# Kernel tuning notes

Hardware: AMD Instinct MI355X
Metric: run time of the kernel (lower is better)

Reference implementation:

```python
import jax, jax.numpy as jnp
import numpy as np

EMBED_DIM = 1024
PROJ_DIM = 128
B = 32
S = 1024


def setup_inputs() -> dict:
    key = jax.random.key(0)
    k1, k2, k3 = jax.random.split(key, 3)
    context = jax.random.normal(k1, (S, B, EMBED_DIM), jnp.float32)  # [seq, batch, embed]
    prior = jax.random.uniform(k2, (B, S), dtype=jnp.float32)
    padding_mask = jnp.zeros((B, S), jnp.int32)
    # xavier_uniform for proj_weight [2*proj_dim, embed_dim]
    bound = float(np.sqrt(6.0 / (2 * PROJ_DIM + EMBED_DIM)))
    proj_weight = jax.random.uniform(k3, (2 * PROJ_DIM, EMBED_DIM), jnp.float32, -bound, bound)
    proj_bias = jnp.zeros((2 * PROJ_DIM,), jnp.float32)
    return {"context": context, "prior": prior, "padding_mask": padding_mask,
            "proj_weight": proj_weight, "proj_bias": proj_bias}


def reference(context, prior, padding_mask, proj_weight, proj_bias):
    ctx = jnp.transpose(context, (1, 0, 2))  # [B, S, E]
    b, s, e = ctx.shape
    qk = ctx @ proj_weight.T + proj_bias  # [B, S, 2*proj_dim]
    query, key = jnp.split(qk, 2, axis=2)
    # neighbor scores (note: original divides by embed_dim, not proj_dim)
    fwd = jnp.sum(query[:, :-1] * key[:, 1:], axis=-1) / e    # [B, S-1]
    bwd = jnp.sum(query[:, 1:] * key[:, :-1], axis=-1) / e    # [B, S-1]
    ninf = jnp.full((b, 1), -jnp.inf, ctx.dtype)
    col0 = jnp.concatenate([fwd, ninf], axis=1)   # score[:, :, 0]
    col1 = jnp.concatenate([ninf, bwd], axis=1)   # score[:, :, 1]
    rolled_mask = jnp.roll(padding_mask, -1, axis=1)
    col0 = jnp.where(rolled_mask == 1, -jnp.inf, col0)
    prob = jax.nn.softmax(jnp.stack([col0, col1], axis=-1), axis=-1)  # [B, S, 2]
    # torch .roll with no dims flattens first -- replicate exactly
    shift_prob = jnp.roll(prob[:, :, 1].reshape(-1), -1).reshape(b, s)
    p = jnp.sqrt(prob[:, :, 0] * shift_prob + 1e-6)
    neighbor_attn = prior + (1 - prior) * p  # [B, S]
    log_prob = jnp.log(neighbor_attn)
    log_prob = jnp.where(rolled_mask == 1, 0.0, log_prob)
    # The two triangular bmms compute C[i,j] = sum_{k=i}^{j-1} log_prob[k] for j>i.
    # Equivalent O(S^2) form via exclusive prefix sum of log_prob[:, :-1].
    csp = jnp.concatenate([jnp.zeros((b, 1), ctx.dtype),
                           jnp.cumsum(log_prob[:, :-1], axis=1)], axis=1)  # [B, S]
    diff = csp[:, None, :] - csp[:, :, None]  # diff[b,i,j] = csp[j] - csp[i]
    upper = jnp.triu(diff, k=1)
    constituent_attn = jnp.exp(upper + jnp.swapaxes(upper, 1, 2))
    constituent_attn = jnp.where(jnp.eye(s, dtype=bool), 0.0, constituent_attn)
    return constituent_attn, neighbor_attn
```

## Files before the change

kernel.cpp:

```cpp
#include <hip/hip_runtime.h>
#include <hip/hip_bf16.h>
#include <math.h>

#define EMB 1024
#define BATCH 32
#define SEQ 1024
#define J2 256
#define BM 64
#define BN 256
#define BK 64
#define NIT (EMB / BK)
#define PSEL 0x07060302u

typedef __attribute__((ext_vector_type(8))) short short8;
typedef __attribute__((ext_vector_type(4))) float f32x4;
typedef const __attribute__((address_space(1))) void gvoid;
typedef __attribute__((address_space(3))) void lvoid;

__device__ __forceinline__ unsigned bcast(float f) {
    union { float f; unsigned u; } c; c.f = f; return c.u;
}
__device__ __forceinline__ unsigned pack_bf16(float f0, float f1) {
    return __builtin_amdgcn_perm(bcast(f1) + 0x8000u, bcast(f0) + 0x8000u, PSEL);
}

__global__ __launch_bounds__(256) void convw(const float* __restrict__ W,
                                             __hip_bfloat16* __restrict__ Wb) {
    int i = blockIdx.x * 256 + threadIdx.x;
    float4 v = ((const float4*)W)[i];
    __hip_bfloat16 h[4];
    h[0] = __float2bfloat16(v.x); h[1] = __float2bfloat16(v.y);
    h[2] = __float2bfloat16(v.z); h[3] = __float2bfloat16(v.w);
    *(short4*)&Wb[i * 4] = *(short4*)h;
}

__global__ __launch_bounds__(256) void gemm_mfma(const float* __restrict__ ctx,
                                                 const __hip_bfloat16* __restrict__ Wb,
                                                 const float* __restrict__ bias,
                                                 __hip_bfloat16* __restrict__ qkb) {
    __shared__ __align__(16) __hip_bfloat16 As[2 * BM * BK];
    __shared__ __align__(16) __hip_bfloat16 Bs[2 * BN * BK];
    const int t = threadIdx.x;
    const int lane = t & 63, w = t >> 6;
    const int m0 = blockIdx.x * BM;
    const int wn = w * 64;
    const int lm = lane & 15, lq = lane >> 4;

    f32x4 acc[4][4] = {};

    float bv[4];
    #pragma unroll
    for (int ni = 0; ni < 4; ni++) bv[ni] = bias[wn + ni * 16 + lm];

    const float4* ctx4 = (const float4*)ctx;
    const int ar0 = t >> 3, ak = t & 7;
    const int ar1 = 32 + ar0;
    const int as0 = (ak ^ (ar0 & 7)) * 8;
    const int as1 = (ak ^ (ar1 & 7)) * 8;
    const size_t abase0 = (size_t)(m0 + ar0) * 256 + ak * 2;
    const size_t abase1 = (size_t)(m0 + ar1) * 256 + ak * 2;

    #pragma unroll
    for (int c = 0; c < 8; c++) {
        int li = c * 256 + t, row = li >> 3;
        int k8 = (li & 7) ^ (row & 7);
        __builtin_amdgcn_global_load_lds(
            (gvoid*)(Wb + (size_t)row * EMB + k8 * 8),
            (lvoid*)&Bs[(c * 256 + w * 64) * 8], 16, 0, 0);
    }
    float4 v0a = ctx4[abase0], v0b = ctx4[abase0 + 1];
    float4 v1a = ctx4[abase1], v1b = ctx4[abase1 + 1];
    {
        uint4 p0, p1;
        p0.x = pack_bf16(v0a.x, v0a.y); p0.y = pack_bf16(v0a.z, v0a.w);
        p0.z = pack_bf16(v0b.x, v0b.y); p0.w = pack_bf16(v0b.z, v0b.w);
        p1.x = pack_bf16(v1a.x, v1a.y); p1.y = pack_bf16(v1a.z, v1a.w);
        p1.z = pack_bf16(v1b.x, v1b.y); p1.w = pack_bf16(v1b.z, v1b.w);
        *(uint4*)&As[ar0 * BK + as0] = p0;
        *(uint4*)&As[ar1 * BK + as1] = p1;
    }
    v0a = ctx4[abase0 + 16]; v0b = ctx4[abase0 + 17];
    v1a = ctx4[abase1 + 16]; v1b = ctx4[abase1 + 17];
    asm volatile("s_waitcnt vmcnt(0) lgkmcnt(0)" ::: "memory");
    __builtin_amdgcn_s_barrier();

    for (int it = 0; it < NIT; ++it) {
        const int cur = it & 1;
        const __hip_bfloat16* Ac = As + cur * (BM * BK);
        const __hip_bfloat16* Bc = Bs + cur * (BN * BK);
        __hip_bfloat16* An = As + (cur ^ 1) * (BM * BK);
        __hip_bfloat16* Bn = Bs + (cur ^ 1) * (BN * BK);
        const bool stage = (it + 1 < NIT);
        const bool pre   = (it + 2 < NIT);
        if (stage) {
            uint4 p0, p1;
            p0.x = pack_bf16(v0a.x, v0a.y); p0.y = pack_bf16(v0a.z, v0a.w);
            p0.z = pack_bf16(v0b.x, v0b.y); p0.w = pack_bf16(v0b.z, v0b.w);
            p1.x = pack_bf16(v1a.x, v1a.y); p1.y = pack_bf16(v1a.z, v1a.w);
            p1.z = pack_bf16(v1b.x, v1b.y); p1.w = pack_bf16(v1b.z, v1b.w);
            *(uint4*)&An[ar0 * BK + as0] = p0;
            *(uint4*)&An[ar1 * BK + as1] = p1;
            const int k0n = (it + 1) * BK;
            #pragma unroll
            for (int c = 0; c < 8; c++) {
                int li = c * 256 + t, row = li >> 3;
                int k8 = (li & 7) ^ (row & 7);
                __builtin_amdgcn_global_load_lds(
                    (gvoid*)(Wb + (size_t)row * EMB + k0n + k8 * 8),
                    (lvoid*)&Bn[(c * 256 + w * 64) * 8], 16, 0, 0);
            }
            if (pre) {
                const size_t ko = (size_t)(it + 2) * (BK / 4);
                v0a = ctx4[abase0 + ko]; v0b = ctx4[abase0 + ko + 1];
                v1a = ctx4[abase1 + ko]; v1b = ctx4[abase1 + ko + 1];
            }
        }
        #pragma unroll
        for (int kk = 0; kk < BK; kk += 32) {
            const int off = ((((kk >> 5) << 2) + lq) ^ (lm & 7)) * 8;
            short8 af[4], bfr[4];
            #pragma unroll
            for (int i = 0; i < 4; i++) {
                af[i]  = *(const short8*)&Ac[(i * 16 + lm) * BK + off];
                bfr[i] = *(const short8*)&Bc[(wn + i * 16 + lm) * BK + off];
            }
            #pragma unroll
            for (int mi = 0; mi < 4; mi++)
                #pragma unroll
                for (int ni = 0; ni < 4; ni++)
                    acc[mi][ni] = __builtin_amdgcn_mfma_f32_16x16x32_bf16(
                        af[mi], bfr[ni], acc[mi][ni], 0, 0, 0);
        }
        if (stage) {
            asm volatile("s_waitcnt vmcnt(0) lgkmcnt(0)" ::: "memory");
            __builtin_amdgcn_s_barrier();
        }
    }

    #pragma unroll
    for (int mi = 0; mi < 4; mi++) {
        #pragma unroll
        for (int r = 0; r < 4; r++) {
            int m = m0 + mi * 16 + lq * 4 + r;
            int s = m >> 5, b = m & 31;
            __hip_bfloat16* orow = qkb + (size_t)((b << 10) + s) * J2;
            #pragma unroll
            for (int ni = 0; ni < 4; ni++) {
                int n = wn + ni * 16 + lm;
                orow[n] = __float2bfloat16(acc[mi][ni][r] + bv[ni]);
            }
        }
    }
}

__global__ __launch_bounds__(256) void scores(const __hip_bfloat16* __restrict__ qkb,
                                              float* __restrict__ fwd,
                                              float* __restrict__ bwd) {
    int wave = threadIdx.x >> 6, lane = threadIdx.x & 63;
    int idx = blockIdx.x * 4 + wave;
    int s = idx & (SEQ - 1);
    if (s == SEQ - 1) return;
    const unsigned* r0 = (const unsigned*)(qkb + (size_t)idx * J2);
    const unsigned* r1 = r0 + 128;
    unsigned q0 = r0[lane], k0 = r0[64 + lane];
    unsigned q1 = r1[lane], k1 = r1[64 + lane];
    float2 q0f = __bfloat1622float2(*(const __hip_bfloat162*)&q0);
    float2 k0f = __bfloat1622float2(*(const __hip_bfloat162*)&k0);
    float2 q1f = __bfloat1622float2(*(const __hip_bfloat162*)&q1);
    float2 k1f = __bfloat1622float2(*(const __hip_bfloat162*)&k1);
    float f = q0f.x * k1f.x + q0f.y * k1f.y;
    float w = q1f.x * k0f.x + q1f.y * k0f.y;
    #pragma unroll
    for (int off = 32; off; off >>= 1) {
        f += __shfl_xor(f, off);
        w += __shfl_xor(w, off);
    }
    if (lane == 0) {
        fwd[idx] = f * (1.f / 1024.f);
        bwd[idx] = w * (1.f / 1024.f);
    }
}

__global__ __launch_bounds__(1024) void neighbor(const float* __restrict__ fwd,
                                                 const float* __restrict__ bwd,
                                                 const float* __restrict__ prior,
                                                 const int* __restrict__ mask,
                                                 float* __restrict__ out_n,
                                                 float* __restrict__ csp) {
    int b = blockIdx.x, s = threadIdx.x;
    int lane = s & 63, w = s >> 6;
    __shared__ float p1s[SEQ];
    __shared__ float incl[SEQ];
    __shared__ float wsum[16];
    int base = b << 10;
    int rolled = mask[base + ((s + 1) & (SEQ - 1))];
    float c0 = (s < SEQ - 1) ? fwd[base + s] : -INFINITY;
    if (rolled) c0 = -INFINITY;
    float c1 = (s > 0) ? bwd[base + s - 1] : -INFINITY;
    float m = fmaxf(c0, c1);
    float e0 = expf(c0 - m), e1 = expf(c1 - m);
    float inv = 1.f / (e0 + e1);
    float p0 = e0 * inv, p1 = e1 * inv;
    p1s[s] = p1;
    __syncthreads();
    float shift = (s < SEQ - 1) ? p1s[s + 1] : 0.f;
    float p = sqrtf(p0 * shift + 1e-6f);
    float pr = prior[base + s];
    float na = pr + (1.f - pr) * p;
    out_n[base + s] = na;
    float lp = logf(na);
    if (rolled) lp = 0.f;
    float x = lp;
    #pragma unroll
    for (int off = 1; off < 64; off <<= 1) {
        float v = __shfl_up(x, off);
        if (lane >= off) x += v;
    }
    if (lane == 63) wsum[w] = x;
    __syncthreads();
    if (w == 0) {
        float v = (lane < 16) ? wsum[lane] : 0.f;
        #pragma unroll
        for (int off = 1; off < 16; off <<= 1) {
            float t2 = __shfl_up(v, off);
            if (lane >= off) v += t2;
        }
        if (lane < 16) wsum[lane] = v;
    }
    __syncthreads();
    float woff = (w > 0) ? wsum[w - 1] : 0.f;
    incl[s] = x + woff;
    __syncthreads();
    csp[base + s] = (s == 0) ? 0.f : incl[s - 1];
}

__global__ __launch_bounds__(256) void outk(const float* __restrict__ csp,
                                            float* __restrict__ out) {
    int blk = blockIdx.x;
    int b = blk >> 7, i0 = (blk & 127) << 3;
    const float* crow = csp + (b << 10);
    int t = threadIdx.x;
    float4 cj = ((const float4*)crow)[t];
    int j0 = t << 2;
    float4* o4 = (float4*)(out + ((size_t)(b << 10) + i0) * SEQ) + t;
    #pragma unroll
    for (int r = 0; r < 8; r++) {
        int i = i0 + r;
        float ci = crow[i];
        float4 v; float d;
        d = (j0 + 0 > i) ? cj.x - ci : ci - cj.x;
        v.x = (j0 + 0 == i) ? 0.f : __expf(d);
        d = (j0 + 1 > i) ? cj.y - ci : ci - cj.y;
        v.y = (j0 + 1 == i) ? 0.f : __expf(d);
        d = (j0 + 2 > i) ? cj.z - ci : ci - cj.z;
        v.z = (j0 + 2 == i) ? 0.f : __expf(d);
        d = (j0 + 3 > i) ? cj.w - ci : ci - cj.w;
        v.w = (j0 + 3 == i) ? 0.f : __expf(d);
        o4[r * 256] = v;
    }
}

extern "C" void kernel_launch(void* const* d_in, const int* in_sizes, int n_in,
                              void* d_out, int out_size, void* d_ws, size_t ws_size,
                              hipStream_t stream) {
    (void)in_sizes; (void)n_in; (void)out_size; (void)ws_size;
    const float* ctx   = (const float*)d_in[0];
    const float* prior = (const float*)d_in[1];
    const int*   mask  = (const int*)d_in[2];
    const float* W     = (const float*)d_in[3];
    const float* bias  = (const float*)d_in[4];
    float* out = (float*)d_out;
    float* ws  = (float*)d_ws;

    __hip_bfloat16* qkb = (__hip_bfloat16*)ws;
    float* fwd = ws + 4194304;
    float* bwd = fwd + 32768;
    float* csp = bwd + 32768;
    __hip_bfloat16* Wb = (__hip_bfloat16*)(csp + 32768);
    float* out_n = out + (size_t)BATCH * SEQ * SEQ;

    convw    <<<256, 256, 0, stream>>>(W, Wb);
    gemm_mfma<<<(BATCH * SEQ) / BM, 256, 0, stream>>>(ctx, Wb, bias, qkb);
    scores   <<<(BATCH * SEQ) / 4, 256, 0, stream>>>(qkb, fwd, bwd);
    neighbor <<<BATCH, 1024, 0, stream>>>(fwd, bwd, prior, mask, out_n, csp);
    outk     <<<(BATCH * SEQ) / 8, 256, 0, stream>>>(csp, out);
}
```

Measured before the change: 269.3 us.

## Read weight fragments directly from global memory instead of staging in LDS

The B operand (bf16 weight) is no longer staged through shared memory with global_load_lds. Each wave now loads its MFMA B fragments straight from global memory, which is expected to hit in L2 since the weight is small and shared by all blocks. The A prefetch distance also drops from two stages to one, and the barrier now waits only on LDS traffic. This cuts LDS use from about 80KB to 16KB, allowing more blocks per CU, but it exposes global-load latency right before the MFMAs and removes the deeper prefetch.

```diff
diff --git a/kernel.cpp b/kernel.cpp
--- a/kernel.cpp
+++ b/kernel.cpp
@@ -14,8 +14,6 @@
 
 typedef __attribute__((ext_vector_type(8))) short short8;
 typedef __attribute__((ext_vector_type(4))) float f32x4;
-typedef const __attribute__((address_space(1))) void gvoid;
-typedef __attribute__((address_space(3))) void lvoid;
 
 __device__ __forceinline__ unsigned bcast(float f) {
     union { float f; unsigned u; } c; c.f = f; return c.u;
@@ -39,7 +37,6 @@
                                                  const float* __restrict__ bias,
                                                  __hip_bfloat16* __restrict__ qkb) {
     __shared__ __align__(16) __hip_bfloat16 As[2 * BM * BK];
-    __shared__ __align__(16) __hip_bfloat16 Bs[2 * BN * BK];
     const int t = threadIdx.x;
     const int lane = t & 63, w = t >> 6;
     const int m0 = blockIdx.x * BM;
@@ -51,6 +48,10 @@
     float bv[4];
     #pragma unroll
     for (int ni = 0; ni < 4; ni++) bv[ni] = bias[wn + ni * 16 + lm];
+
+    const __hip_bfloat16* bp[4];
+    #pragma unroll
+    for (int ni = 0; ni < 4; ni++) bp[ni] = Wb + (size_t)(wn + ni * 16 + lm) * EMB;
 
     const float4* ctx4 = (const float4*)ctx;
     const int ar0 = t >> 3, ak = t & 7;
@@ -60,17 +61,9 @@
     const size_t abase0 = (size_t)(m0 + ar0) * 256 + ak * 2;
     const size_t abase1 = (size_t)(m0 + ar1) * 256 + ak * 2;
 
-    #pragma unroll
-    for (int c = 0; c < 8; c++) {
-        int li = c * 256 + t, row = li >> 3;
-        int k8 = (li & 7) ^ (row & 7);
-        __builtin_amdgcn_global_load_lds(
-            (gvoid*)(Wb + (size_t)row * EMB + k8 * 8),
-            (lvoid*)&Bs[(c * 256 + w * 64) * 8], 16, 0, 0);
-    }
-    float4 v0a = ctx4[abase0], v0b = ctx4[abase0 + 1];
-    float4 v1a = ctx4[abase1], v1b = ctx4[abase1 + 1];
     {
+        float4 v0a = ctx4[abase0], v0b = ctx4[abase0 + 1];
+        float4 v1a = ctx4[abase1], v1b = ctx4[abase1 + 1];
         uint4 p0, p1;
         p0.x = pack_bf16(v0a.x, v0a.y); p0.y = pack_bf16(v0a.z, v0a.w);
         p0.z = pack_bf16(v0b.x, v0b.y); p0.w = pack_bf16(v0b.z, v0b.w);
@@ -79,19 +72,38 @@
         *(uint4*)&As[ar0 * BK + as0] = p0;
         *(uint4*)&As[ar1 * BK + as1] = p1;
     }
-    v0a = ctx4[abase0 + 16]; v0b = ctx4[abase0 + 17];
-    v1a = ctx4[abase1 + 16]; v1b = ctx4[abase1 + 17];
-    asm volatile("s_waitcnt vmcnt(0) lgkmcnt(0)" ::: "memory");
+    asm volatile("s_waitcnt lgkmcnt(0)" ::: "memory");
     __builtin_amdgcn_s_barrier();
 
     for (int it = 0; it < NIT; ++it) {
         const int cur = it & 1;
         const __hip_bfloat16* Ac = As + cur * (BM * BK);
-        const __hip_bfloat16* Bc = Bs + cur * (BN * BK);
         __hip_bfloat16* An = As + (cur ^ 1) * (BM * BK);
-        __hip_bfloat16* Bn = Bs + (cur ^ 1) * (BN * BK);
         const bool stage = (it + 1 < NIT);
-        const bool pre   = (it + 2 < NIT);
+        const int k0 = it * BK;
+        float4 v0a, v0b, v1a, v1b;
+        if (stage) {
+            const size_t ko = (size_t)(it + 1) * (BK / 4);
+            v0a = ctx4[abase0 + ko]; v0b = ctx4[abase0 + ko + 1];
+            v1a = ctx4[abase1 + ko]; v1b = ctx4[abase1 + ko + 1];
+        }
+        #pragma unroll
+        for (int kk = 0; kk < BK; kk += 32) {
+            const int off = ((((kk >> 5) << 2) + lq) ^ (lm & 7)) * 8;
+            const int bo = k0 + kk + lq * 8;
+            short8 af[4], bfr[4];
+            #pragma unroll
+            for (int i = 0; i < 4; i++) {
+                af[i]  = *(const short8*)&Ac[(i * 16 + lm) * BK + off];
+                bfr[i] = *(const short8*)(bp[i] + bo);
+            }
+            #pragma unroll
+            for (int mi = 0; mi < 4; mi++)
+                #pragma unroll
+                for (int ni = 0; ni < 4; ni++)
+                    acc[mi][ni] = __builtin_amdgcn_mfma_f32_16x16x32_bf16(
+                        af[mi], bfr[ni], acc[mi][ni], 0, 0, 0);
+        }
         if (stage) {
             uint4 p0, p1;
             p0.x = pack_bf16(v0a.x, v0a.y); p0.y = pack_bf16(v0a.z, v0a.w);
@@ -100,39 +112,7 @@
             p1.z = pack_bf16(v1b.x, v1b.y); p1.w = pack_bf16(v1b.z, v1b.w);
             *(uint4*)&An[ar0 * BK + as0] = p0;
             *(uint4*)&An[ar1 * BK + as1] = p1;
-            const int k0n = (it + 1) * BK;
-            #pragma unroll
-            for (int c = 0; c < 8; c++) {
-                int li = c * 256 + t, row = li >> 3;
-                int k8 = (li & 7) ^ (row & 7);
-                __builtin_amdgcn_global_load_lds(
-                    (gvoid*)(Wb + (size_t)row * EMB + k0n + k8 * 8),
-                    (lvoid*)&Bn[(c * 256 + w * 64) * 8], 16, 0, 0);
-            }
-            if (pre) {
-                const size_t ko = (size_t)(it + 2) * (BK / 4);
-                v0a = ctx4[abase0 + ko]; v0b = ctx4[abase0 + ko + 1];
-                v1a = ctx4[abase1 + ko]; v1b = ctx4[abase1 + ko + 1];
-            }
-        }
-        #pragma unroll
-        for (int kk = 0; kk < BK; kk += 32) {
-            const int off = ((((kk >> 5) << 2) + lq) ^ (lm & 7)) * 8;
-            short8 af[4], bfr[4];
-            #pragma unroll
-            for (int i = 0; i < 4; i++) {
-                af[i]  = *(const short8*)&Ac[(i * 16 + lm) * BK + off];
-                bfr[i] = *(const short8*)&Bc[(wn + i * 16 + lm) * BK + off];
-            }
-            #pragma unroll
-            for (int mi = 0; mi < 4; mi++)
-                #pragma unroll
-                for (int ni = 0; ni < 4; ni++)
-                    acc[mi][ni] = __builtin_amdgcn_mfma_f32_16x16x32_bf16(
-                        af[mi], bfr[ni], acc[mi][ni], 0, 0, 0);
-        }
-        if (stage) {
-            asm volatile("s_waitcnt vmcnt(0) lgkmcnt(0)" ::: "memory");
+            asm volatile("s_waitcnt lgkmcnt(0)" ::: "memory");
             __builtin_amdgcn_s_barrier();
         }
     }
```

Measured after the change: 275.7 us. 1.02x slower.

## Halve GEMM tile to BM=32, BK=32 with in-loop A prefetch

Applied to the files above, without the earlier changes.

Shrinks the projection GEMM tile from 64 to 32 rows and the K step from 64 to 32, with a new LDS swizzle for 4 chunks per row. This doubles the number of blocks to fill more CUs. The A-tile prefetch now loads one iteration ahead inside the loop and writes to LDS after the MFMAs, replacing the two-deep register prefetch. The cost is more barriers and K iterations, and the 256-wide weight tile is reloaded by twice as many blocks.

```diff
diff --git a/kernel.cpp b/kernel.cpp
--- a/kernel.cpp
+++ b/kernel.cpp
@@ -6,9 +6,9 @@
 #define BATCH 32
 #define SEQ 1024
 #define J2 256
-#define BM 64
+#define BM 32
 #define BN 256
-#define BK 64
+#define BK 32
 #define NIT (EMB / BK)
 #define PSEL 0x07060302u
 
@@ -46,41 +46,33 @@
     const int wn = w * 64;
     const int lm = lane & 15, lq = lane >> 4;
 
-    f32x4 acc[4][4] = {};
+    f32x4 acc[2][4] = {};
 
     float bv[4];
     #pragma unroll
     for (int ni = 0; ni < 4; ni++) bv[ni] = bias[wn + ni * 16 + lm];
 
     const float4* ctx4 = (const float4*)ctx;
-    const int ar0 = t >> 3, ak = t & 7;
-    const int ar1 = 32 + ar0;
-    const int as0 = (ak ^ (ar0 & 7)) * 8;
-    const int as1 = (ak ^ (ar1 & 7)) * 8;
-    const size_t abase0 = (size_t)(m0 + ar0) * 256 + ak * 2;
-    const size_t abase1 = (size_t)(m0 + ar1) * 256 + ak * 2;
-
-    #pragma unroll
-    for (int c = 0; c < 8; c++) {
-        int li = c * 256 + t, row = li >> 3;
-        int k8 = (li & 7) ^ (row & 7);
+    const bool astage = (t < 128);
+    const int ar = t >> 2, ak = t & 3;
+    const int aslot = (ak ^ ((ar >> 1) & 3)) * 8;
+    const size_t abase = (size_t)(m0 + ar) * 256 + ak * 2;
+
+    #pragma unroll
+    for (int c = 0; c < 4; c++) {
+        int li = c * 256 + t, row = li >> 2;
+        int k8 = (li & 3) ^ ((row >> 1) & 3);
         __builtin_amdgcn_global_load_lds(
             (gvoid*)(Wb + (size_t)row * EMB + k8 * 8),
             (lvoid*)&Bs[(c * 256 + w * 64) * 8], 16, 0, 0);
     }
-    float4 v0a = ctx4[abase0], v0b = ctx4[abase0 + 1];
-    float4 v1a = ctx4[abase1], v1b = ctx4[abase1 + 1];
-    {
-        uint4 p0, p1;
-        p0.x = pack_bf16(v0a.x, v0a.y); p0.y = pack_bf16(v0a.z, v0a.w);
-        p0.z = pack_bf16(v0b.x, v0b.y); p0.w = pack_bf16(v0b.z, v0b.w);
-        p1.x = pack_bf16(v1a.x, v1a.y); p1.y = pack_bf16(v1a.z, v1a.w);
-        p1.z = pack_bf16(v1b.x, v1b.y); p1.w = pack_bf16(v1b.z, v1b.w);
-        *(uint4*)&As[ar0 * BK + as0] = p0;
-        *(uint4*)&As[ar1 * BK + as1] = p1;
-    }
-    v0a = ctx4[abase0 + 16]; v0b = ctx4[abase0 + 17];
-    v1a = ctx4[abase1 + 16]; v1b = ctx4[abase1 + 17];
+    if (astage) {
+        float4 va = ctx4[abase], vb = ctx4[abase + 1];
+        uint4 p;
+        p.x = pack_bf16(va.x, va.y); p.y = pack_bf16(va.z, va.w);
+        p.z = pack_bf16(vb.x, vb.y); p.w = pack_bf16(vb.z, vb.w);
+        *(uint4*)&As[ar * BK + aslot] = p;
+    }
     asm volatile("s_waitcnt vmcnt(0) lgkmcnt(0)" ::: "memory");
     __builtin_amdgcn_s_barrier();
 
@@ -91,54 +83,52 @@
         __hip_bfloat16* An = As + (cur ^ 1) * (BM * BK);
         __hip_bfloat16* Bn = Bs + (cur ^ 1) * (BN * BK);
         const bool stage = (it + 1 < NIT);
-        const bool pre   = (it + 2 < NIT);
+        float4 va = {}, vb = {};
         if (stage) {
-            uint4 p0, p1;
-            p0.x = pack_bf16(v0a.x, v0a.y); p0.y = pack_bf16(v0a.z, v0a.w);
-            p0.z = pack_bf16(v0b.x, v0b.y); p0.w = pack_bf16(v0b.z, v0b.w);
-            p1.x = pack_bf16(v1a.x, v1a.y); p1.y = pack_bf16(v1a.z, v1a.w);
-            p1.z = pack_bf16(v1b.x, v1b.y); p1.w = pack_bf16(v1b.z, v1b.w);
-            *(uint4*)&An[ar0 * BK + as0] = p0;
-            *(uint4*)&An[ar1 * BK + as1] = p1;
+            if (astage) {
+                const size_t ko = (size_t)(it + 1) * (BK / 4);
+                va = ctx4[abase + ko]; vb = ctx4[abase + ko + 1];
+            }
             const int k0n = (it + 1) * BK;
             #pragma unroll
-            for (int c = 0; c < 8; c++) {
-                int li = c * 256 + t, row = li >> 3;
-                int k8 = (li & 7) ^ (row & 7);
+            for (int c = 0; c < 4; c++) {
+                int li = c * 256 + t, row = li >> 2;
+                int k8 = (li & 3) ^ ((row >> 1) & 3);
                 __builtin_amdgcn_global_load_lds(
                     (gvoid*)(Wb + (size_t)row * EMB + k0n + k8 * 8),
                     (lvoid*)&Bn[(c * 256 + w * 64) * 8], 16, 0, 0);
             }
-            if (pre) {
-                const size_t ko = (size_t)(it + 2) * (BK / 4);
-                v0a = ctx4[abase0 + ko]; v0b = ctx4[abase0 + ko + 1];
-                v1a = ctx4[abase1 + ko]; v1b = ctx4[abase1 + ko + 1];
-            }
-        }
-        #pragma unroll
-        for (int kk = 0; kk < BK; kk += 32) {
-            const int off = ((((kk >> 5) << 2) + lq) ^ (lm & 7)) * 8;
-            short8 af[4], bfr[4];
-            #pragma unroll
-            for (int i = 0; i < 4; i++) {
-                af[i]  = *(const short8*)&Ac[(i * 16 + lm) * BK + off];
+        }
+        {
+            const int off = (lq ^ ((lm >> 1) & 3)) * 8;
+            short8 af[2], bfr[4];
+            #pragma unroll
+            for (int i = 0; i < 2; i++)
+                af[i] = *(const short8*)&Ac[(i * 16 + lm) * BK + off];
+            #pragma unroll
+            for (int i = 0; i < 4; i++)
                 bfr[i] = *(const short8*)&Bc[(wn + i * 16 + lm) * BK + off];
-            }
-            #pragma unroll
-            for (int mi = 0; mi < 4; mi++)
+            #pragma unroll
+            for (int mi = 0; mi < 2; mi++)
                 #pragma unroll
                 for (int ni = 0; ni < 4; ni++)
                     acc[mi][ni] = __builtin_amdgcn_mfma_f32_16x16x32_bf16(
                         af[mi], bfr[ni], acc[mi][ni], 0, 0, 0);
         }
         if (stage) {
+            if (astage) {
+                uint4 p;
+                p.x = pack_bf16(va.x, va.y); p.y = pack_bf16(va.z, va.w);
+                p.z = pack_bf16(vb.x, vb.y); p.w = pack_bf16(vb.z, vb.w);
+                *(uint4*)&An[ar * BK + aslot] = p;
+            }
             asm volatile("s_waitcnt vmcnt(0) lgkmcnt(0)" ::: "memory");
             __builtin_amdgcn_s_barrier();
         }
     }
 
     #pragma unroll
-    for (int mi = 0; mi < 4; mi++) {
+    for (int mi = 0; mi < 2; mi++) {
         #pragma unroll
         for (int r = 0; r < 4; r++) {
             int m = m0 + mi * 16 + lq * 4 + r;
```

Result: slower. 294.3 us (+9.3%).
